# Optimization experiments

Hardware: AMD Instinct MI355X
Metric: run time of the kernel (lower is better)

## Reference

```python
import jax, jax.numpy as jnp
import numpy as np

B, P, D = 8, 1024, 768
H = 12
HD = D // H


def setup_inputs() -> dict:
    key = jax.random.key(0)
    k1, k2, k3, k4, k5 = jax.random.split(key, 5)
    s = 0.02
    return {
        "x": jax.random.normal(k1, (B, P, D), dtype=jnp.float32),
        "w_qkv": jax.random.normal(k2, (D, 3 * D), dtype=jnp.float32) * s,
        "b_qkv": jax.random.normal(k3, (3 * D,), dtype=jnp.float32) * s,
        "w_proj": jax.random.normal(k4, (D, D), dtype=jnp.float32) * s,
        "b_proj": jax.random.normal(k5, (D,), dtype=jnp.float32) * s,
    }


def reference(x, w_qkv, b_qkv, w_proj, b_proj):
    b, p, d = x.shape
    scale = HD ** -0.5
    qkv = x @ w_qkv + b_qkv                      # [B,P,3D]
    qkv = qkv.reshape(b, p, 3, H, HD).transpose(2, 0, 3, 1, 4)  # [3,B,H,P,HD]
    q, k, v = qkv[0], qkv[1], qkv[2]
    attn = jnp.einsum("bhqd,bhkd->bhqk", q, k) * scale
    attn = jax.nn.softmax(attn, axis=-1)         # attn_drop is identity (p=0)
    weighted_avg = jnp.einsum("bhqk,bhkd->bhqd", attn, v)
    weighted_avg = weighted_avg.transpose(0, 2, 1, 3).reshape(b, p, d)  # [B,P,D]
    out = weighted_avg @ w_proj + b_proj         # proj_drop is identity (p=0)
    return (out, weighted_avg)
```

## Files before the change

kernel.cpp:

```cpp
#include <hip/hip_runtime.h>
#include <hip/hip_bf16.h>


typedef __attribute__((ext_vector_type(8))) short short8;
typedef __attribute__((ext_vector_type(4))) float f32x4;

#define MFMA_BF16(a, b, c) __builtin_amdgcn_mfma_f32_16x16x32_bf16((a), (b), (c), 0, 0, 0)

#define NB 8
#define NP 1024
#define ND 768
#define NH 12
#define NHD 64
#define NTOK (NB * NP)
#define N3D (3 * ND)
#define OUT_HALF (NTOK * ND)
#define QSCALE 0.18033688f

__device__ __forceinline__ void gload_lds16(const void* gptr, void* ldsptr) {
  __builtin_amdgcn_global_load_lds(
      (const __attribute__((address_space(1))) unsigned int*)gptr,
      (__attribute__((address_space(3))) unsigned int*)ldsptr, 16, 0, 0);
}

__device__ __forceinline__ unsigned pack_bf16x2(float a, float b) {
  __hip_bfloat162 h = __float22bfloat162_rn(float2{a, b});
  return *reinterpret_cast<unsigned*>(&h);
}

__device__ __forceinline__ int swz_g(int b) { return b ^ (((b >> 7) & 7) << 4); }


__global__ void k_cvt_x(const float* __restrict__ in, __hip_bfloat16* __restrict__ out) {
  int i = (blockIdx.x * 256 + threadIdx.x) * 8;
  float4 a = *(const float4*)(in + i);
  float4 b = *(const float4*)(in + i + 4);
  union { __hip_bfloat16 h[8]; uint4 u; } r;
  r.h[0] = __float2bfloat16(a.x); r.h[1] = __float2bfloat16(a.y);
  r.h[2] = __float2bfloat16(a.z); r.h[3] = __float2bfloat16(a.w);
  r.h[4] = __float2bfloat16(b.x); r.h[5] = __float2bfloat16(b.y);
  r.h[6] = __float2bfloat16(b.z); r.h[7] = __float2bfloat16(b.w);
  *(uint4*)(out + i) = r.u;
}

__global__ void k_cvt_t(const float* __restrict__ in, __hip_bfloat16* __restrict__ out,
                        int K, int N) {
  __shared__ float tile[32][33];
  int k0 = blockIdx.x * 32;
  int n0 = blockIdx.y * 32;
  int r = threadIdx.x >> 5;
  int c = threadIdx.x & 31;
#pragma unroll
  for (int i = 0; i < 4; ++i)
    tile[r + 8 * i][c] = in[(size_t)(k0 + r + 8 * i) * N + n0 + c];
  __syncthreads();
#pragma unroll
  for (int i = 0; i < 4; ++i)
    out[(size_t)(n0 + r + 8 * i) * K + k0 + c] = __float2bfloat16(tile[c][r + 8 * i]);
}


__device__ __forceinline__ void gemm_mainloop(const __hip_bfloat16* __restrict__ A,
                                              const __hip_bfloat16* __restrict__ BT,
                                              int m0, int n0, char* Ls,
                                              f32x4 acc[4][4]) {
  const int tid = threadIdx.x;
  const int wid = tid >> 6, lane = tid & 63;
  const int wm = wid >> 1, wn = wid & 1;
  const int lrow = lane & 15, lk = lane >> 4;
  constexpr int K = 768, NKT = K / 64;

  int aoff[4][2], boff[4][2];
#pragma unroll
  for (int i = 0; i < 4; ++i)
#pragma unroll
    for (int kh = 0; kh < 2; ++kh) {
      aoff[i][kh] = swz_g((wm * 64 + i * 16 + lrow) * 128 + kh * 64 + lk * 16);
      boff[i][kh] = swz_g((wn * 64 + i * 16 + lrow) * 128 + kh * 64 + lk * 16);
    }

#define STAGE_G(kt, bi)                                                  \
  {                                                                      \
    const int k0s = (kt) * 64;                                           \
    char* dst = Ls + (bi) * 32768;                                       \
    _Pragma("unroll")                                                    \
    for (int t = 0; t < 4; ++t) {                                        \
      const int L = t * 4096 + tid * 16;           \
      const int lb = swz_g(L);                         \
      const int mr = lb >> 7;                  \
      const int kk = (lb & 127) >> 1;           \
      gload_lds16(A + (size_t)(m0 + mr) * K + k0s + kk, dst + L);        \
      gload_lds16(BT + (size_t)(n0 + mr) * K + k0s + kk,                 \
                  dst + 16384 + L);                                      \
    }                                                                    \
  }

  STAGE_G(0, 0);
  STAGE_G(1, 1);

#pragma unroll 2
  for (int kt = 0; kt < NKT - 1; ++kt) {
    asm volatile("s_waitcnt vmcnt(8)" ::: "memory");
    __builtin_amdgcn_s_barrier();

    const char* buf = Ls + (kt & 1) * 32768;
    short8 af[4][2], bf[4][2];
#pragma unroll
    for (int i = 0; i < 4; ++i)
#pragma unroll
      for (int kh = 0; kh < 2; ++kh) {
        af[i][kh] = *(const short8*)(buf + aoff[i][kh]);
        bf[i][kh] = *(const short8*)(buf + 16384 + boff[i][kh]);
      }

    asm volatile("s_waitcnt lgkmcnt(0)" ::: "memory");
    __builtin_amdgcn_s_barrier();

    if (kt + 2 < NKT) STAGE_G(kt + 2, kt & 1);

#pragma unroll
    for (int kh = 0; kh < 2; ++kh)
#pragma unroll
      for (int mi = 0; mi < 4; ++mi)
#pragma unroll
        for (int ni = 0; ni < 4; ++ni)
          acc[mi][ni] = MFMA_BF16(af[mi][kh], bf[ni][kh], acc[mi][ni]);
  }

  asm volatile("s_waitcnt vmcnt(0)" ::: "memory");
  __builtin_amdgcn_s_barrier();
  {
    const char* buf = Ls + ((NKT - 1) & 1) * 32768;
    short8 af[4][2], bf[4][2];
#pragma unroll
    for (int i = 0; i < 4; ++i)
#pragma unroll
      for (int kh = 0; kh < 2; ++kh) {
        af[i][kh] = *(const short8*)(buf + aoff[i][kh]);
        bf[i][kh] = *(const short8*)(buf + 16384 + boff[i][kh]);
      }
#pragma unroll
    for (int kh = 0; kh < 2; ++kh)
#pragma unroll
      for (int mi = 0; mi < 4; ++mi)
#pragma unroll
        for (int ni = 0; ni < 4; ++ni)
          acc[mi][ni] = MFMA_BF16(af[mi][kh], bf[ni][kh], acc[mi][ni]);
  }
#undef STAGE_G
}


__launch_bounds__(256)
__global__ void k_qkv_gemm(const __hip_bfloat16* __restrict__ A,
                           const __hip_bfloat16* __restrict__ BT,
                           const float* __restrict__ bias,
                           __hip_bfloat16* __restrict__ q_ws,
                           __hip_bfloat16* __restrict__ k_ws,
                           __hip_bfloat16* __restrict__ v_ws) {
  __shared__ char Ls[2 * 32768];
  const int mt = blockIdx.x & 63, nt = blockIdx.x >> 6;
  const int m0 = mt * 128, n0 = nt * 128;
  const int wid = threadIdx.x >> 6, lane = threadIdx.x & 63;
  const int wm = wid >> 1, wn = wid & 1;
  const int lrow = lane & 15, lk = lane >> 4;

  f32x4 acc[4][4] = {};
  gemm_mainloop(A, BT, m0, n0, Ls, acc);

  const int which = n0 / ND;
#pragma unroll
  for (int ni = 0; ni < 4; ++ni) {
    const int n = n0 + wn * 64 + ni * 16 + lrow;
    const float bv = bias[n];
    const int hh = (n % ND) >> 6;
    const int hd = n & 63;
#pragma unroll
    for (int mi = 0; mi < 4; ++mi) {
      const int mbase = m0 + wm * 64 + mi * 16 + lk * 4;
#pragma unroll
      for (int i = 0; i < 4; ++i) {
        const int m = mbase + i;
        const float v = acc[mi][ni][i] + bv;
        const int b = m >> 10, p = m & 1023;
        const int bh = b * NH + hh;
        if (which == 0)      q_ws[((size_t)bh * NP + p) * NHD + hd] = __float2bfloat16(v * QSCALE);
        else if (which == 1) k_ws[((size_t)bh * NP + p) * NHD + hd] = __float2bfloat16(v);
        else                 v_ws[((size_t)bh * NHD + hd) * NP + p] = __float2bfloat16(v);
      }
    }
  }
}


#define KVBLK 64

__launch_bounds__(128)
__global__ void k_attn(const __hip_bfloat16* __restrict__ q_ws,
                       const __hip_bfloat16* __restrict__ k_ws,
                       const __hip_bfloat16* __restrict__ v_ws,
                       float* __restrict__ wavg_f32,
                       __hip_bfloat16* __restrict__ wavg_bf) {
  __shared__ char smem[2 * 16384 + 2 * 9216];
  const int bid = blockIdx.x;
  const int wg = (bid & 7) * 96 + (bid >> 3);
  const int bh = wg >> 3, qb = wg & 7;
  const int tid = threadIdx.x;
  const int wid = tid >> 6, lane = tid & 63;
  const int lrow = lane & 15, lk = lane >> 4;
  const int q0 = qb * 128 + wid * 64;
  char* pbuf = smem + 32768 + wid * 9216;

  const __hip_bfloat16* Qb = q_ws + (size_t)bh * NP * NHD;
  const __hip_bfloat16* Kb = k_ws + (size_t)bh * NP * NHD;
  const __hip_bfloat16* Vb = v_ws + (size_t)bh * NHD * NP;

  short8 qf[4][2];
#pragma unroll
  for (int g = 0; g < 4; ++g) {
    qf[g][0] = *(const short8*)(Qb + (size_t)(q0 + g * 16 + lrow) * NHD + lk * 8);
    qf[g][1] = *(const short8*)(Qb + (size_t)(q0 + g * 16 + lrow) * NHD + 32 + lk * 8);
  }

  f32x4 acc[4][4] = {};
  float dsum[4] = {0.f, 0.f, 0.f, 0.f};

#define STAGE(buf, key0)                                                          \
  {                                                                               \
    _Pragma("unroll")                                                             \
    for (int p = 0; p < 4; ++p) {                                                 \
      const int L = p * 2048 + tid * 16;                                          \
      const int r = L >> 7;                                                       \
      const int cb = L & 127;                                                     \
      const int sc = (cb ^ ((r & 7) << 4)) >> 1;        \
      gload_lds16(Kb + (size_t)((key0) + r) * NHD + sc, (buf) + L);               \
      gload_lds16(Vb + (size_t)r * NP + (key0) + sc, (buf) + 8192 + L);           \
    }                                                                             \
  }

  char* cur = smem;
  char* nxt = smem + 16384;
  STAGE(cur, 0);
  __syncthreads();

  for (int kc = 0; kc < NP / KVBLK; ++kc) {
    if (kc < NP / KVBLK - 1) STAGE(nxt, (kc + 1) * KVBLK);

    char* Ks = cur;
    char* Vs = cur + 8192;

#pragma unroll
    for (int kt = 0; kt < 4; ++kt) {
      const int row = kt * 16 + lrow;
      const int sw = (row & 7) << 4;
      short8 klo = *(const short8*)(Ks + row * 128 + ((lk * 16) ^ sw));
      short8 khi = *(const short8*)(Ks + row * 128 + ((64 + lk * 16) ^ sw));
      f32x4 s[4];
      __builtin_amdgcn_s_setprio(1);
#pragma unroll
      for (int g = 0; g < 4; ++g) {
        f32x4 z = {0.f, 0.f, 0.f, 0.f};
        s[g] = MFMA_BF16(klo, qf[g][0], z);
        s[g] = MFMA_BF16(khi, qf[g][1], s[g]);
      }
      __builtin_amdgcn_s_setprio(0);
#pragma unroll
      for (int g = 0; g < 4; ++g) {
        const float p0 = __builtin_amdgcn_exp2f(s[g][0]);
        const float p1 = __builtin_amdgcn_exp2f(s[g][1]);
        const float p2 = __builtin_amdgcn_exp2f(s[g][2]);
        const float p3 = __builtin_amdgcn_exp2f(s[g][3]);
        dsum[g] += (p0 + p1) + (p2 + p3);
        uint2 w;
        w.x = pack_bf16x2(p0, p1);
        w.y = pack_bf16x2(p2, p3);
        *(uint2*)(pbuf + (g * 16 + lrow) * 144 + kt * 32 + lk * 8) = w;
      }
    }

#pragma unroll
    for (int kh = 0; kh < 2; ++kh) {
      short8 a2[4];
#pragma unroll
      for (int g = 0; g < 4; ++g)
        a2[g] = *(const short8*)(pbuf + (g * 16 + lrow) * 144 + kh * 64 + lk * 16);
      __builtin_amdgcn_s_setprio(1);
#pragma unroll
      for (int hdt = 0; hdt < 4; ++hdt) {
        const int row = hdt * 16 + lrow;
        short8 vf = *(const short8*)(Vs + row * 128 +
                                     ((kh * 64 + lk * 16) ^ ((row & 7) << 4)));
#pragma unroll
        for (int g = 0; g < 4; ++g)
          acc[g][hdt] = MFMA_BF16(a2[g], vf, acc[g][hdt]);
      }
      __builtin_amdgcn_s_setprio(0);
    }

    __syncthreads();
    char* t = cur; cur = nxt; nxt = t;
  }

  const int b = bh / NH, hh = bh % NH;
#pragma unroll
  for (int g = 0; g < 4; ++g) {
    float ds = dsum[g];
    ds += __shfl_xor(ds, 16);
    ds += __shfl_xor(ds, 32);
    float rd[4];
#pragma unroll
    for (int i = 0; i < 4; ++i) rd[i] = 1.0f / __shfl(ds, lk * 4 + i, 16);

#pragma unroll
    for (int hdt = 0; hdt < 4; ++hdt) {
#pragma unroll
      for (int i = 0; i < 4; ++i) {
        const int qq = q0 + g * 16 + lk * 4 + i;
        const int col = hh * NHD + hdt * 16 + lrow;
        const float val = acc[g][hdt][i] * rd[i];
        const size_t o = ((size_t)b * NP + qq) * ND + col;
        wavg_f32[o] = val;
        wavg_bf[o] = __float2bfloat16(val);
      }
    }
  }
#undef STAGE
}


__launch_bounds__(256)
__global__ void k_proj_gemm(const __hip_bfloat16* __restrict__ A,
                            const __hip_bfloat16* __restrict__ BT,
                            const float* __restrict__ bias,
                            float* __restrict__ C) {
  __shared__ char Ls[2 * 32768];
  const int mt = blockIdx.x & 63, nt = blockIdx.x >> 6;
  const int m0 = mt * 128, n0 = nt * 128;
  const int wid = threadIdx.x >> 6, lane = threadIdx.x & 63;
  const int wm = wid >> 1, wn = wid & 1;
  const int lrow = lane & 15, lk = lane >> 4;

  f32x4 acc[4][4] = {};
  gemm_mainloop(A, BT, m0, n0, Ls, acc);

#pragma unroll
  for (int ni = 0; ni < 4; ++ni) {
    const int n = n0 + wn * 64 + ni * 16 + lrow;
    const float bv = bias[n];
#pragma unroll
    for (int mi = 0; mi < 4; ++mi) {
      const int mbase = m0 + wm * 64 + mi * 16 + lk * 4;
#pragma unroll
      for (int i = 0; i < 4; ++i)
        C[(size_t)(mbase + i) * ND + n] = acc[mi][ni][i] + bv;
    }
  }
}


extern "C" void kernel_launch(void* const* d_in, const int* in_sizes, int n_in,
                              void* d_out, int out_size, void* d_ws, size_t ws_size,
                              hipStream_t stream) {
  const float* x      = (const float*)d_in[0];
  const float* w_qkv  = (const float*)d_in[1];
  const float* b_qkv  = (const float*)d_in[2];
  const float* w_proj = (const float*)d_in[3];
  const float* b_proj = (const float*)d_in[4];
  float* out = (float*)d_out;
  float* wavg_out = out + OUT_HALF;

  char* ws = (char*)d_ws;
  __hip_bfloat16* xbf    = (__hip_bfloat16*)(ws);
  __hip_bfloat16* wqkvT  = (__hip_bfloat16*)(ws + 12582912);
  __hip_bfloat16* wprojT = (__hip_bfloat16*)(ws + 16121856);
  __hip_bfloat16* q_ws   = (__hip_bfloat16*)(ws + 17301504);
  __hip_bfloat16* k_ws   = (__hip_bfloat16*)(ws + 29884416);
  __hip_bfloat16* v_ws   = (__hip_bfloat16*)(ws + 42467328);
  __hip_bfloat16* wavg_bf = xbf;

  k_cvt_x<<<NTOK * ND / (256 * 8), 256, 0, stream>>>(x, xbf);
  k_cvt_t<<<dim3(ND / 32, N3D / 32), 256, 0, stream>>>(w_qkv, wqkvT, ND, N3D);
  k_cvt_t<<<dim3(ND / 32, ND / 32), 256, 0, stream>>>(w_proj, wprojT, ND, ND);
  k_qkv_gemm<<<(NTOK / 128) * (N3D / 128), 256, 0, stream>>>(xbf, wqkvT, b_qkv,
                                                             q_ws, k_ws, v_ws);
  k_attn<<<(NP / 128) * (NB * NH), 128, 0, stream>>>(q_ws, k_ws, v_ws, wavg_out, wavg_bf);
  k_proj_gemm<<<(NTOK / 128) * (ND / 128), 256, 0, stream>>>(wavg_bf, wprojT, b_proj, out);
}
```

Measured before the change: 132.7 us.

## Enlarge proj GEMM tile to 256x128 with 512 threads and interleave attention QK/PV

The projection GEMM moves to 256x128 tiles with 8 waves, a dedicated double-buffered pipeline that keeps two stages in flight, and a remapped block index meant to improve cache locality. In the attention kernel, the score/exp computation for each half of the key block is interleaved with the matching PV MFMAs, so the PV work can start before all four key tiles are done. The larger tile needs 96KB LDS and fewer blocks (192), which may reduce occupancy and CU coverage.

```diff
diff --git a/kernel.cpp b/kernel.cpp
--- a/kernel.cpp
+++ b/kernel.cpp
@@ -250,36 +250,37 @@
     char* Vs = cur + 8192;
 
 #pragma unroll
-    for (int kt = 0; kt < 4; ++kt) {
-      const int row = kt * 16 + lrow;
-      const int sw = (row & 7) << 4;
-      short8 klo = *(const short8*)(Ks + row * 128 + ((lk * 16) ^ sw));
-      short8 khi = *(const short8*)(Ks + row * 128 + ((64 + lk * 16) ^ sw));
-      f32x4 s[4];
-      __builtin_amdgcn_s_setprio(1);
-#pragma unroll
-      for (int g = 0; g < 4; ++g) {
-        f32x4 z = {0.f, 0.f, 0.f, 0.f};
-        s[g] = MFMA_BF16(klo, qf[g][0], z);
-        s[g] = MFMA_BF16(khi, qf[g][1], s[g]);
-      }
-      __builtin_amdgcn_s_setprio(0);
-#pragma unroll
-      for (int g = 0; g < 4; ++g) {
-        const float p0 = __builtin_amdgcn_exp2f(s[g][0]);
-        const float p1 = __builtin_amdgcn_exp2f(s[g][1]);
-        const float p2 = __builtin_amdgcn_exp2f(s[g][2]);
-        const float p3 = __builtin_amdgcn_exp2f(s[g][3]);
-        dsum[g] += (p0 + p1) + (p2 + p3);
-        uint2 w;
-        w.x = pack_bf16x2(p0, p1);
-        w.y = pack_bf16x2(p2, p3);
-        *(uint2*)(pbuf + (g * 16 + lrow) * 144 + kt * 32 + lk * 8) = w;
-      }
-    }
-
-#pragma unroll
     for (int kh = 0; kh < 2; ++kh) {
+#pragma unroll
+      for (int ktl = 0; ktl < 2; ++ktl) {
+        const int kt = kh * 2 + ktl;
+        const int row = kt * 16 + lrow;
+        const int sw = (row & 7) << 4;
+        short8 klo = *(const short8*)(Ks + row * 128 + ((lk * 16) ^ sw));
+        short8 khi = *(const short8*)(Ks + row * 128 + ((64 + lk * 16) ^ sw));
+        f32x4 s[4];
+        __builtin_amdgcn_s_setprio(1);
+#pragma unroll
+        for (int g = 0; g < 4; ++g) {
+          f32x4 z = {0.f, 0.f, 0.f, 0.f};
+          s[g] = MFMA_BF16(klo, qf[g][0], z);
+          s[g] = MFMA_BF16(khi, qf[g][1], s[g]);
+        }
+        __builtin_amdgcn_s_setprio(0);
+#pragma unroll
+        for (int g = 0; g < 4; ++g) {
+          const float p0 = __builtin_amdgcn_exp2f(s[g][0]);
+          const float p1 = __builtin_amdgcn_exp2f(s[g][1]);
+          const float p2 = __builtin_amdgcn_exp2f(s[g][2]);
+          const float p3 = __builtin_amdgcn_exp2f(s[g][3]);
+          dsum[g] += (p0 + p1) + (p2 + p3);
+          uint2 w;
+          w.x = pack_bf16x2(p0, p1);
+          w.y = pack_bf16x2(p2, p3);
+          *(uint2*)(pbuf + (g * 16 + lrow) * 144 + kt * 32 + lk * 8) = w;
+        }
+      }
+
       short8 a2[4];
 #pragma unroll
       for (int g = 0; g < 4; ++g)
@@ -328,20 +329,108 @@
 }
 
 
-__launch_bounds__(256)
+__launch_bounds__(512)
 __global__ void k_proj_gemm(const __hip_bfloat16* __restrict__ A,
                             const __hip_bfloat16* __restrict__ BT,
                             const float* __restrict__ bias,
                             float* __restrict__ C) {
-  __shared__ char Ls[2 * 32768];
-  const int mt = blockIdx.x & 63, nt = blockIdx.x >> 6;
-  const int m0 = mt * 128, n0 = nt * 128;
-  const int wid = threadIdx.x >> 6, lane = threadIdx.x & 63;
+  __shared__ char Ls[2 * 49152];
+  constexpr int K = 768, NKT = K / 64;
+  const int bid = blockIdx.x;
+  const int wg = (bid & 7) * 24 + (bid >> 3);
+  const int mt = wg & 31, nt = wg >> 5;
+  const int m0 = mt * 256, n0 = nt * 128;
+  const int tid = threadIdx.x;
+  const int wid = tid >> 6, lane = tid & 63;
   const int wm = wid >> 1, wn = wid & 1;
   const int lrow = lane & 15, lk = lane >> 4;
 
+  int aoff[4][2], boff[4][2];
+#pragma unroll
+  for (int i = 0; i < 4; ++i)
+#pragma unroll
+    for (int kh = 0; kh < 2; ++kh) {
+      aoff[i][kh] = swz_g((wm * 64 + i * 16 + lrow) * 128 + kh * 64 + lk * 16);
+      boff[i][kh] = swz_g((wn * 64 + i * 16 + lrow) * 128 + kh * 64 + lk * 16);
+    }
+
+#define STAGE_P(kt, bi)                                                  \
+  {                                                                      \
+    const int k0s = (kt) * 64;                                           \
+    char* dst = Ls + (bi) * 49152;                                       \
+    _Pragma("unroll")                                                    \
+    for (int t = 0; t < 4; ++t) {                          \
+      const int L = t * 8192 + tid * 16;                                 \
+      const int lb = swz_g(L);                                           \
+      gload_lds16(A + (size_t)(m0 + (lb >> 7)) * K + k0s +               \
+                      ((lb & 127) >> 1),                                 \
+                  dst + L);                                              \
+    }                                                                    \
+    _Pragma("unroll")                                                    \
+    for (int t = 0; t < 2; ++t) {                          \
+      const int L = t * 8192 + tid * 16;                                 \
+      const int lb = swz_g(L);                                           \
+      gload_lds16(BT + (size_t)(n0 + (lb >> 7)) * K + k0s +              \
+                       ((lb & 127) >> 1),                                \
+                  dst + 32768 + L);                                      \
+    }                                                                    \
+  }
+
+  STAGE_P(0, 0);
+  STAGE_P(1, 1);
+
   f32x4 acc[4][4] = {};
-  gemm_mainloop(A, BT, m0, n0, Ls, acc);
+
+#pragma unroll 2
+  for (int kt = 0; kt < NKT - 1; ++kt) {
+    asm volatile("s_waitcnt vmcnt(6)" ::: "memory");
+    __builtin_amdgcn_s_barrier();
+
+    const char* buf = Ls + (kt & 1) * 49152;
+    short8 af[4][2], bf[4][2];
+#pragma unroll
+    for (int i = 0; i < 4; ++i)
+#pragma unroll
+      for (int kh = 0; kh < 2; ++kh) {
+        af[i][kh] = *(const short8*)(buf + aoff[i][kh]);
+        bf[i][kh] = *(const short8*)(buf + 32768 + boff[i][kh]);
+      }
+
+    asm volatile("s_waitcnt lgkmcnt(0)" ::: "memory");
+    __builtin_amdgcn_s_barrier();
+
+    if (kt + 2 < NKT) STAGE_P(kt + 2, kt & 1);
+
+#pragma unroll
+    for (int kh = 0; kh < 2; ++kh)
+#pragma unroll
+      for (int mi = 0; mi < 4; ++mi)
+#pragma unroll
+        for (int ni = 0; ni < 4; ++ni)
+          acc[mi][ni] = MFMA_BF16(af[mi][kh], bf[ni][kh], acc[mi][ni]);
+  }
+
+  asm volatile("s_waitcnt vmcnt(0)" ::: "memory");
+  __builtin_amdgcn_s_barrier();
+  {
+    const char* buf = Ls + ((NKT - 1) & 1) * 49152;
+    short8 af[4][2], bf[4][2];
+#pragma unroll
+    for (int i = 0; i < 4; ++i)
+#pragma unroll
+      for (int kh = 0; kh < 2; ++kh) {
+        af[i][kh] = *(const short8*)(buf + aoff[i][kh]);
+        bf[i][kh] = *(const short8*)(buf + 32768 + boff[i][kh]);
+      }
+#pragma unroll
+    for (int kh = 0; kh < 2; ++kh)
+#pragma unroll
+      for (int mi = 0; mi < 4; ++mi)
+#pragma unroll
+        for (int ni = 0; ni < 4; ++ni)
+          acc[mi][ni] = MFMA_BF16(af[mi][kh], bf[ni][kh], acc[mi][ni]);
+  }
+#undef STAGE_P
 
 #pragma unroll
   for (int ni = 0; ni < 4; ++ni) {
@@ -384,5 +473,5 @@
   k_qkv_gemm<<<(NTOK / 128) * (N3D / 128), 256, 0, stream>>>(xbf, wqkvT, b_qkv,
                                                              q_ws, k_ws, v_ws);
   k_attn<<<(NP / 128) * (NB * NH), 128, 0, stream>>>(q_ws, k_ws, v_ws, wavg_out, wavg_bf);
-  k_proj_gemm<<<(NTOK / 128) * (ND / 128), 256, 0, stream>>>(wavg_bf, wprojT, b_proj, out);
-}
+  k_proj_gemm<<<(NTOK / 256) * (ND / 128), 512, 0, stream>>>(wavg_bf, wprojT, b_proj, out);
+}
```

Result: slower. 137.6 us (+3.7%).
